# Kernel tuning notes

Hardware: AMD Instinct MI355X
Metric: run time of the kernel (lower is better)

Reference implementation:

```python
import jax, jax.numpy as jnp
import numpy as np

B, S, D = 8, 2048, 512  # batch, seq_len, dim_val == dim_attn

def setup_inputs() -> dict:
    key = jax.random.key(0)
    kx, kq, kk, kv = jax.random.split(key, 4)
    scale = 1.0 / np.sqrt(D)
    return {
        "x": jax.random.normal(kx, (B, S, D), dtype=jnp.float32),
        "Wq": jax.random.normal(kq, (D, D), dtype=jnp.float32) * scale,  # dim_input -> dim_attn
        "Wk": jax.random.normal(kk, (D, D), dtype=jnp.float32) * scale,
        "Wv": jax.random.normal(kv, (D, D), dtype=jnp.float32) * scale,  # dim_input -> dim_val
    }

def reference(x, Wq, Wk, Wv):
    # bias-free linear projections (nn.Linear stores W as [out,in]; here W is [in,out])
    Q = jnp.einsum("bsd,de->bse", x, Wq)
    K = jnp.einsum("bsd,de->bse", x, Wk)
    V = jnp.einsum("bsd,de->bse", x, Wv)
    # manual scaled dot-product attention: softmax(QK^T / sqrt(d_attn)) V
    scores = jnp.einsum("bqe,bke->bqk", Q, K) / jnp.sqrt(jnp.asarray(Q.shape[-1], Q.dtype))
    a = jax.nn.softmax(scores, axis=-1)
    return jnp.einsum("bqk,bkd->bqd", a, V)
```

## Files before the change

### kernel.cpp

```cpp
#include <hip/hip_runtime.h>


typedef __attribute__((ext_vector_type(8))) short bf16x8;
typedef __attribute__((ext_vector_type(4))) short short4v;
typedef __attribute__((ext_vector_type(4))) float f32x4;
typedef __attribute__((ext_vector_type(16))) float f32x16;

__device__ __forceinline__ short f2bf(float f) {
  union { float f; unsigned u; } v; v.f = f;
  unsigned r = v.u + 0x7fffu + ((v.u >> 16) & 1u);
  return (short)(r >> 16);
}

__device__ __forceinline__ float exp2_raw(float x) {
  float r;
  asm("v_exp_f32 %0, %1" : "=v"(r) : "v"(x));
  return r;
}

__device__ __forceinline__ void async_cp16(const void* g, void* l) {
  __builtin_amdgcn_global_load_lds(
      (const __attribute__((address_space(1))) unsigned int*)g,
      (__attribute__((address_space(3))) unsigned int*)l, 16, 0, 0);
}

__global__ __launch_bounds__(256) void prep_kernel(const float* __restrict__ x,
                                                   const float* __restrict__ Wq,
                                                   const float* __restrict__ Wk,
                                                   const float* __restrict__ Wv,
                                                   short* __restrict__ WT,
                                                   short* __restrict__ xb) {
  if (blockIdx.x < 384) {
    int g = blockIdx.x * 256 + threadIdx.x;
    int w = g >> 15;
    int rem = g & 32767;
    int n = rem & 511;
    int k0 = (rem >> 9) << 3;
    const float* W = (w == 0) ? Wq : ((w == 1) ? Wk : Wv);
    bf16x8 o;
#pragma unroll
    for (int j = 0; j < 8; ++j) o[j] = f2bf(W[(k0 + j) * 512 + n]);
    *(bf16x8*)(WT + w * 262144 + n * 512 + k0) = o;
  } else {
    size_t g = (size_t)(blockIdx.x - 384) * 256 + threadIdx.x;
    size_t off = g * 8;
    f32x4 lo = *(const f32x4*)(x + off);
    f32x4 hi = *(const f32x4*)(x + off + 4);
    bf16x8 o;
    o[0] = f2bf(lo[0]); o[1] = f2bf(lo[1]); o[2] = f2bf(lo[2]); o[3] = f2bf(lo[3]);
    o[4] = f2bf(hi[0]); o[5] = f2bf(hi[1]); o[6] = f2bf(hi[2]); o[7] = f2bf(hi[3]);
    *(bf16x8*)(xb + off) = o;
  }
}

__global__ __launch_bounds__(256, 3) void proj_kernel(const short* __restrict__ xb,
                                                      const short* __restrict__ WT,
                                                      short* __restrict__ QP,
                                                      short* __restrict__ KP,
                                                      short* __restrict__ VP) {
  __shared__ __align__(16) short smem[10240];
  short* Af = smem;
  short* Bf = smem + 4096;
  short* Tb = smem;

  const int tid = threadIdx.x, wv = tid >> 6, ln = tid & 63;
  const int lane_m = ln & 15, lane_q = ln >> 4;
  const int m0 = blockIdx.x * 128, n0 = blockIdx.y * 64;
  const int wm = wv & 1, wn = wv >> 1;

  f32x4 zero4 = {0.f, 0.f, 0.f, 0.f};
  f32x4 acc[3][4][2];
#pragma unroll
  for (int z = 0; z < 3; ++z)
#pragma unroll
    for (int i = 0; i < 4; ++i)
#pragma unroll
      for (int j = 0; j < 2; ++j) acc[z][i][j] = zero4;

#pragma unroll 1
  for (int kk = 0; kk < 16; ++kk) {
    const int k0 = kk * 32;
    __syncthreads();
#pragma unroll
    for (int i = 0; i < 2; ++i) {
      const int mt = wv * 2 + i;
      async_cp16(xb + (size_t)(m0 + mt * 16 + lane_m) * 512 + k0 + lane_q * 8, Af + mt * 512);
    }
#pragma unroll
    for (int z = 0; z < 3; ++z)
      async_cp16(WT + z * 262144 + (size_t)(n0 + wv * 16 + lane_m) * 512 + k0 + lane_q * 8,
                 Bf + z * 2048 + wv * 512);
    __syncthreads();
    bf16x8 a[4];
#pragma unroll
    for (int mi = 0; mi < 4; ++mi) a[mi] = *(bf16x8*)(Af + ((wm * 4 + mi) * 512) + ln * 8);
#pragma unroll
    for (int z = 0; z < 3; ++z) {
      bf16x8 b0 = *(bf16x8*)(Bf + z * 2048 + (wn * 2 + 0) * 512 + ln * 8);
      bf16x8 b1 = *(bf16x8*)(Bf + z * 2048 + (wn * 2 + 1) * 512 + ln * 8);
#pragma unroll
      for (int mi = 0; mi < 4; ++mi) {
        acc[z][mi][0] = __builtin_amdgcn_mfma_f32_16x16x32_bf16(a[mi], b0, acc[z][mi][0], 0, 0, 0);
        acc[z][mi][1] = __builtin_amdgcn_mfma_f32_16x16x32_bf16(a[mi], b1, acc[z][mi][1], 0, 0, 0);
      }
    }
  }

  const int bb = m0 >> 11;

#pragma unroll
  for (int z = 0; z < 2; ++z) {
    __syncthreads();
#pragma unroll
    for (int mi = 0; mi < 4; ++mi)
#pragma unroll
      for (int nj = 0; nj < 2; ++nj)
#pragma unroll
        for (int rr = 0; rr < 4; ++rr)
          Tb[(wm * 64 + mi * 16 + lane_q * 4 + rr) * 68 + wn * 32 + nj * 16 + lane_m] =
              f2bf(acc[z][mi][nj][rr]);
    __syncthreads();
    short* Odst = (z == 0) ? QP : KP;
    const int g0 = (m0 & 2047) >> 5, kst0 = n0 >> 4;
#pragma unroll
    for (int p = 0; p < 4; ++p) {
      const int c2 = p * 256 + tid;
      const int frag = c2 >> 6, ln2 = c2 & 63;
      const int gl = frag >> 2, kl = frag & 3;
      const short* src = Tb + (gl * 32 + (ln2 & 31)) * 68 + kl * 16 + ((ln2 >> 5) << 3);
      size_t dst = (size_t)bb * 1048576 + (size_t)((g0 + gl) * 32 + kst0 + kl) * 512 + ln2 * 8;
      *(bf16x8*)(Odst + dst) = *(const bf16x8*)src;
    }
  }
  {
    __syncthreads();
#pragma unroll
    for (int mi = 0; mi < 4; ++mi)
#pragma unroll
      for (int nj = 0; nj < 2; ++nj)
#pragma unroll
        for (int rr = 0; rr < 4; ++rr)
          Tb[(wn * 32 + nj * 16 + lane_m) * 132 + wm * 64 + mi * 16 + lane_q * 4 + rr] =
              f2bf(acc[2][mi][nj][rr]);
    __syncthreads();
    const int ng0 = n0 >> 5, kv0 = (m0 & 2047) >> 4;
#pragma unroll
    for (int p = 0; p < 4; ++p) {
      const int c2 = p * 256 + tid;
      const int frag = c2 >> 6, ln2 = c2 & 63;
      const int ngl = frag >> 3, kvl = frag & 7;
      const short* src = Tb + (ngl * 32 + (ln2 & 31)) * 132 + kvl * 16 + ((ln2 >> 5) << 3);
      size_t dst = (size_t)bb * 1048576 + (size_t)((ng0 + ngl) * 128 + kv0 + kvl) * 512 + ln2 * 8;
      *(bf16x8*)(VP + dst) = *(const bf16x8*)src;
    }
  }
}


#define ISSUE8(R, a0_, a1_, B)                                               \
  asm volatile("global_load_dwordx4 %0, %8, %10\n\t"                         \
               "global_load_dwordx4 %1, %8, %10 offset:1024\n\t"             \
               "global_load_dwordx4 %2, %8, %10 offset:2048\n\t"             \
               "global_load_dwordx4 %3, %8, %10 offset:3072\n\t"             \
               "global_load_dwordx4 %4, %9, %10\n\t"                         \
               "global_load_dwordx4 %5, %9, %10 offset:1024\n\t"             \
               "global_load_dwordx4 %6, %9, %10 offset:2048\n\t"             \
               "global_load_dwordx4 %7, %9, %10 offset:3072\n\t"             \
               : "=&v"(R[0]), "=&v"(R[1]), "=&v"(R[2]), "=&v"(R[3]),         \
                 "=&v"(R[4]), "=&v"(R[5]), "=&v"(R[6]), "=&v"(R[7])          \
               : "v"(a0_), "v"(a1_), "s"(B))

#define WAIT8(R, N)                                                          \
  asm volatile("s_waitcnt vmcnt(" #N ")"                                     \
               : "+v"(R[0]), "+v"(R[1]), "+v"(R[2]), "+v"(R[3]),             \
                 "+v"(R[4]), "+v"(R[5]), "+v"(R[6]), "+v"(R[7]))

#define MFMA32(A, B, C) __builtin_amdgcn_mfma_f32_32x32x16_bf16(A, B, C, 0, 0, 0)

#define ISSUE_KQ(X, kt_, qq)                                                 \
  { const unsigned a0 = kb0 + (unsigned)(((kt_) & 7) * 262144) + (qq) * 8192u; \
    ISSUE8(X, a0, a0 + 4096u, Kp); }

#define ISSUE_VQ(X, kt_, bb_)                                                \
  { const unsigned a0 = vb0 + (unsigned)((kt_) * 16384) + (bb_) * 4096u;     \
    ISSUE8(X, a0, a0 + 131072u, VTp); }

#define S_PHASE(X, ph)                                                       \
  WAIT8(X, 8);                                                               \
  __builtin_amdgcn_s_setprio(1);                                             \
  _Pragma("unroll")                                                          \
  for (int c = 0; c < 8; ++c) {                                              \
    const int kst = (ph) * 8 + c;                                            \
    bf16x8 q0 = *(bf16x8*)(qf + kst * 512 + ln * 8);                         \
    bf16x8 q1 = *(bf16x8*)(qf + (32 + kst) * 512 + ln * 8);                  \
    s0 = MFMA32(X[c], q0, s0);                                               \
    s1 = MFMA32(X[c], q1, s1);                                               \
  }                                                                          \
  __builtin_amdgcn_s_setprio(0);

#define PF_RD(qh_, kv_)                                                      \
  (*(bf16x8*)(pfb + (qh_) * 8192 + q32 * 256 + ((((kv_) * 16) + hq8) ^ sw3)))

#define PV_PHASE(X, bb_)                                                     \
  WAIT8(X, 8);                                                               \
  __builtin_amdgcn_s_setprio(1);                                             \
  _Pragma("unroll")                                                          \
  for (int c = 0; c < 4; ++c) {                                              \
    const int kv = (bb_) * 4 + c;                                            \
    bf16x8 p0 = PF_RD(0, kv);                                                \
    bf16x8 p1 = PF_RD(1, kv);                                                \
    O00 = MFMA32(X[c], p0, O00);                                             \
    O01 = MFMA32(X[c], p1, O01);                                             \
    O10 = MFMA32(X[4 + c], p0, O10);                                         \
    O11 = MFMA32(X[4 + c], p1, O11);                                         \
  }                                                                          \
  __builtin_amdgcn_s_setprio(0);

__global__ __launch_bounds__(512, 2) void flash_kernel(const short* __restrict__ Q,
                                                       const short* __restrict__ K,
                                                       const short* __restrict__ VT,
                                                       float* __restrict__ out) {
  __shared__ __align__(16) short qf[32768];
  __shared__ __align__(16) short pf[32768];
  __shared__ float l_red[8][64];
  __shared__ float lsum[64];

  const int tid = threadIdx.x, w = tid >> 6, ln = tid & 63;
  const int q32 = ln & 31, hq = ln >> 5;
  const int hq8 = hq * 8, hq4 = hq * 4;
  const int sw3 = (q32 & 7) << 3;
  const int b = blockIdx.x & 7, qt = blockIdx.x >> 3;
  const int m0 = qt * 64;
  const short* Qp = Q + (size_t)b * 1048576;
  const short* Kp = K + (size_t)b * 1048576;
  const short* VTp = VT + (size_t)b * 1048576;
  const float sc2 = 0.044194173824159216f * 1.4426950408889634f;

#pragma unroll
  for (int r = 0; r < 8; ++r) {
    const int reg = w * 8 + r;
    *(bf16x8*)(qf + reg * 512 + ln * 8) =
        *(const bf16x8*)(Qp + (size_t)(qt * 64 + reg) * 512 + ln * 8);
  }

  f32x16 zz = {};
  f32x16 O00 = zz, O01 = zz, O10 = zz, O11 = zz;
  float lp0 = 0.f, lp1 = 0.f;

  const unsigned kb0 = (unsigned)(w * 32768 + ln * 16);
  const unsigned vb0 = (unsigned)(w * 262144 + ln * 16);

  __syncthreads();

  bf16x8 kX[8], kY[8], vA[8], vB[8];
  ISSUE_KQ(kX, 0, 0);
  ISSUE_KQ(kY, 0, 1);

#pragma unroll 1
  for (int kt = 0; kt < 8; ++kt) {
    f32x16 s0 = zz, s1 = zz;
    short* pfb = pf + (kt & 1) * 16384;

    S_PHASE(kX, 0); ISSUE_KQ(kX, kt, 2);
    S_PHASE(kY, 1); ISSUE_KQ(kY, kt, 3);
    S_PHASE(kX, 2); ISSUE_VQ(vA, kt, 0);
    S_PHASE(kY, 3); ISSUE_VQ(vB, kt, 1);

#pragma unroll
    for (int g2 = 0; g2 < 4; ++g2) {
      float a0 = exp2_raw(s0[g2 * 4 + 0] * sc2 - 12.0f);
      float a1 = exp2_raw(s0[g2 * 4 + 1] * sc2 - 12.0f);
      float a2 = exp2_raw(s0[g2 * 4 + 2] * sc2 - 12.0f);
      float a3 = exp2_raw(s0[g2 * 4 + 3] * sc2 - 12.0f);
      lp0 += (a0 + a1) + (a2 + a3);
      short4v v0c = {f2bf(a0), f2bf(a1), f2bf(a2), f2bf(a3)};
      *(short4v*)(pfb + q32 * 256 + (((w * 32 + g2 * 8) + hq4) ^ sw3)) = v0c;
      float c0 = exp2_raw(s1[g2 * 4 + 0] * sc2 - 12.0f);
      float c1 = exp2_raw(s1[g2 * 4 + 1] * sc2 - 12.0f);
      float c2 = exp2_raw(s1[g2 * 4 + 2] * sc2 - 12.0f);
      float c3 = exp2_raw(s1[g2 * 4 + 3] * sc2 - 12.0f);
      lp1 += (c0 + c1) + (c2 + c3);
      short4v v1c = {f2bf(c0), f2bf(c1), f2bf(c2), f2bf(c3)};
      *(short4v*)(pfb + 8192 + q32 * 256 + (((w * 32 + g2 * 8) + hq4) ^ sw3)) = v1c;
    }
    asm volatile("s_waitcnt lgkmcnt(0)" ::: "memory");
    __builtin_amdgcn_s_barrier();
    asm volatile("" ::: "memory");

    PV_PHASE(vA, 0); ISSUE_VQ(vA, kt, 2);
    PV_PHASE(vB, 1); ISSUE_VQ(vB, kt, 3);
    PV_PHASE(vA, 2); ISSUE_KQ(kX, kt + 1, 0);
    PV_PHASE(vB, 3); ISSUE_KQ(kY, kt + 1, 1);
  }
  WAIT8(kX, 8);
  WAIT8(kY, 0);

  lp0 += __shfl_xor(lp0, 32);
  lp1 += __shfl_xor(lp1, 32);
  if (ln < 32) {
    l_red[w][q32] = lp0;
    l_red[w][32 + q32] = lp1;
  }
  __syncthreads();
  if (tid < 64) {
    float s = 0.f;
#pragma unroll
    for (int ww = 0; ww < 8; ++ww) s += l_red[ww][tid];
    lsum[tid] = s;
  }
  __syncthreads();

  const float li0 = 1.f / lsum[q32];
  const float li1 = 1.f / lsum[32 + q32];
#pragma unroll
  for (int g2 = 0; g2 < 4; ++g2) {
    const int dq = g2 * 8 + hq4;
    const size_t r0 = ((size_t)b * 2048 + m0 + q32) * 512 + w * 64;
    const size_t r1 = ((size_t)b * 2048 + m0 + 32 + q32) * 512 + w * 64;
    f32x4 o;
    o[0] = O00[g2 * 4 + 0] * li0; o[1] = O00[g2 * 4 + 1] * li0;
    o[2] = O00[g2 * 4 + 2] * li0; o[3] = O00[g2 * 4 + 3] * li0;
    *(f32x4*)(out + r0 + dq) = o;
    o[0] = O10[g2 * 4 + 0] * li0; o[1] = O10[g2 * 4 + 1] * li0;
    o[2] = O10[g2 * 4 + 2] * li0; o[3] = O10[g2 * 4 + 3] * li0;
    *(f32x4*)(out + r0 + 32 + dq) = o;
    o[0] = O01[g2 * 4 + 0] * li1; o[1] = O01[g2 * 4 + 1] * li1;
    o[2] = O01[g2 * 4 + 2] * li1; o[3] = O01[g2 * 4 + 3] * li1;
    *(f32x4*)(out + r1 + dq) = o;
    o[0] = O11[g2 * 4 + 0] * li1; o[1] = O11[g2 * 4 + 1] * li1;
    o[2] = O11[g2 * 4 + 2] * li1; o[3] = O11[g2 * 4 + 3] * li1;
    *(f32x4*)(out + r1 + 32 + dq) = o;
  }
}

extern "C" void kernel_launch(void* const* d_in, const int* in_sizes, int n_in,
                              void* d_out, int out_size, void* d_ws, size_t ws_size,
                              hipStream_t stream) {
  const float* x  = (const float*)d_in[0];
  const float* Wq = (const float*)d_in[1];
  const float* Wk = (const float*)d_in[2];
  const float* Wv = (const float*)d_in[3];
  float* out = (float*)d_out;
  char* ws = (char*)d_ws;
  short* WT = (short*)ws;
  short* QP = (short*)(ws + 1572864);
  short* KP = (short*)(ws + 1572864 + 16777216);
  short* VP = (short*)(ws + 1572864 + 2 * 16777216);
  short* xb = (short*)(ws + 1572864 + 3 * 16777216);

  prep_kernel<<<dim3(384 + 4096), dim3(256), 0, stream>>>(x, Wq, Wk, Wv, WT, xb);
  proj_kernel<<<dim3(128, 8), dim3(256), 0, stream>>>(xb, WT, QP, KP, VP);
  flash_kernel<<<dim3(256), dim3(512), 0, stream>>>(QP, KP, VP, out);
}
```

Measured before the change: 210.0 us.

## Load projection GEMM operands directly from global into registers, drop LDS staging

The QKV projection kernel no longer stages x and W tiles through shared memory with async global-to-LDS copies and two barriers per k-step. Each wave now loads its MFMA operand fragments straight from global memory into registers, with precomputed pointers and a fully unrolled k loop that lets the compiler overlap loads with MFMAs. Launch bounds drop to 2 blocks per SM to allow more registers. The cost is redundant global/L2 reads, since operands are no longer shared across waves, and lower occupancy.

```diff
diff --git a/kernel.cpp b/kernel.cpp
--- a/kernel.cpp
+++ b/kernel.cpp
@@ -16,12 +16,6 @@
   float r;
   asm("v_exp_f32 %0, %1" : "=v"(r) : "v"(x));
   return r;
-}
-
-__device__ __forceinline__ void async_cp16(const void* g, void* l) {
-  __builtin_amdgcn_global_load_lds(
-      (const __attribute__((address_space(1))) unsigned int*)g,
-      (__attribute__((address_space(3))) unsigned int*)l, 16, 0, 0);
 }
 
 __global__ __launch_bounds__(256) void prep_kernel(const float* __restrict__ x,
@@ -53,21 +47,29 @@
   }
 }
 
-__global__ __launch_bounds__(256, 3) void proj_kernel(const short* __restrict__ xb,
+__global__ __launch_bounds__(256, 2) void proj_kernel(const short* __restrict__ xb,
                                                       const short* __restrict__ WT,
                                                       short* __restrict__ QP,
                                                       short* __restrict__ KP,
                                                       short* __restrict__ VP) {
-  __shared__ __align__(16) short smem[10240];
-  short* Af = smem;
-  short* Bf = smem + 4096;
-  short* Tb = smem;
+  __shared__ __align__(16) short Tb[8704];
 
   const int tid = threadIdx.x, wv = tid >> 6, ln = tid & 63;
   const int lane_m = ln & 15, lane_q = ln >> 4;
   const int m0 = blockIdx.x * 128, n0 = blockIdx.y * 64;
   const int wm = wv & 1, wn = wv >> 1;
 
+  const short* ap[4];
+#pragma unroll
+  for (int mi = 0; mi < 4; ++mi)
+    ap[mi] = xb + (size_t)(m0 + (wm * 4 + mi) * 16 + lane_m) * 512 + lane_q * 8;
+  const short* bp[3][2];
+#pragma unroll
+  for (int z = 0; z < 3; ++z)
+#pragma unroll
+    for (int nj = 0; nj < 2; ++nj)
+      bp[z][nj] = WT + z * 262144 + (size_t)(n0 + (wn * 2 + nj) * 16 + lane_m) * 512 + lane_q * 8;
+
   f32x4 zero4 = {0.f, 0.f, 0.f, 0.f};
   f32x4 acc[3][4][2];
 #pragma unroll
@@ -77,33 +79,24 @@
 #pragma unroll
       for (int j = 0; j < 2; ++j) acc[z][i][j] = zero4;
 
-#pragma unroll 1
+#pragma unroll
   for (int kk = 0; kk < 16; ++kk) {
-    const int k0 = kk * 32;
-    __syncthreads();
-#pragma unroll
-    for (int i = 0; i < 2; ++i) {
-      const int mt = wv * 2 + i;
-      async_cp16(xb + (size_t)(m0 + mt * 16 + lane_m) * 512 + k0 + lane_q * 8, Af + mt * 512);
-    }
+    const int ko = kk * 32;
+    bf16x8 a[4];
+#pragma unroll
+    for (int mi = 0; mi < 4; ++mi) a[mi] = *(const bf16x8*)(ap[mi] + ko);
+    bf16x8 b[3][2];
 #pragma unroll
     for (int z = 0; z < 3; ++z)
-      async_cp16(WT + z * 262144 + (size_t)(n0 + wv * 16 + lane_m) * 512 + k0 + lane_q * 8,
-                 Bf + z * 2048 + wv * 512);
-    __syncthreads();
-    bf16x8 a[4];
-#pragma unroll
-    for (int mi = 0; mi < 4; ++mi) a[mi] = *(bf16x8*)(Af + ((wm * 4 + mi) * 512) + ln * 8);
-#pragma unroll
-    for (int z = 0; z < 3; ++z) {
-      bf16x8 b0 = *(bf16x8*)(Bf + z * 2048 + (wn * 2 + 0) * 512 + ln * 8);
-      bf16x8 b1 = *(bf16x8*)(Bf + z * 2048 + (wn * 2 + 1) * 512 + ln * 8);
+#pragma unroll
+      for (int nj = 0; nj < 2; ++nj) b[z][nj] = *(const bf16x8*)(bp[z][nj] + ko);
+#pragma unroll
+    for (int z = 0; z < 3; ++z)
 #pragma unroll
       for (int mi = 0; mi < 4; ++mi) {
-        acc[z][mi][0] = __builtin_amdgcn_mfma_f32_16x16x32_bf16(a[mi], b0, acc[z][mi][0], 0, 0, 0);
-        acc[z][mi][1] = __builtin_amdgcn_mfma_f32_16x16x32_bf16(a[mi], b1, acc[z][mi][1], 0, 0, 0);
+        acc[z][mi][0] = __builtin_amdgcn_mfma_f32_16x16x32_bf16(a[mi], b[z][0], acc[z][mi][0], 0, 0, 0);
+        acc[z][mi][1] = __builtin_amdgcn_mfma_f32_16x16x32_bf16(a[mi], b[z][1], acc[z][mi][1], 0, 0, 0);
       }
-    }
   }
 
   const int bb = m0 >> 11;
```

New measurement: 234.0 us. 1.11x slower.
